# Kernel tuning notes

Measured on AMD Instinct MI355X. Metric: run time of the kernel, lower is better.

The kernel has to match this reference:

```python
import jax, jax.numpy as jnp
import numpy as np

N_HEADS = 16
D_MODEL = 1024
D_HEAD = 64
B, S = 4, 2048


def setup_inputs() -> dict:
    key = jax.random.key(0)
    kv, kk, kq, kwi, kwo = jax.random.split(key, 5)
    v = jax.random.normal(kv, (B, S, D_MODEL), dtype=jnp.float32)
    k = jax.random.normal(kk, (B, S, D_MODEL), dtype=jnp.float32)
    q = jax.random.normal(kq, (B, S, D_MODEL), dtype=jnp.float32)
    wi = jax.random.normal(kwi, (D_MODEL, D_HEAD), dtype=jnp.float32) * (D_MODEL ** -0.5)
    Wo = jax.random.normal(kwo, (N_HEADS * D_HEAD, D_MODEL), dtype=jnp.float32) * ((N_HEADS * D_HEAD) ** -0.5)
    bo = jnp.zeros((D_MODEL,), dtype=jnp.float32)
    return {"v": v, "k": k, "q": q, "wi": wi, "Wo": Wo, "bo": bo}


def reference(v, k, q, wi, Wo, bo):
    # Every head shares the same wi and has no params -> all head outputs are identical.
    # Compute the single head once, then tile n_heads times (matches jnp.concatenate of copies).
    qp = q @ wi  # [B,S,Dh]
    kp = k @ wi
    vp = v @ wi
    scores = jnp.einsum("bsd,btd->bst", qp, kp) / jnp.sqrt(jnp.asarray(D_HEAD, qp.dtype))
    attn = jax.nn.softmax(scores, axis=-1)  # [B,S,S]
    head = qp + jnp.einsum("bst,btd->bsd", attn, vp)  # residual q + attn@v, [B,S,Dh]
    concat = jnp.tile(head, (1, 1, N_HEADS))  # [B,S,n_heads*Dh]
    return concat @ Wo + bo  # Dense(d_model)
```

## Files before the change

kernel.cpp:

```cpp
#include <hip/hip_runtime.h>

typedef __bf16 bf16x8 __attribute__((ext_vector_type(8)));
typedef float f32x4 __attribute__((ext_vector_type(4)));
typedef unsigned short ushort8 __attribute__((ext_vector_type(8)));
typedef unsigned short ushort4v __attribute__((ext_vector_type(4)));

#define S_LEN 2048
#define DMODEL 1024
#define DHEAD 64
#define QK_SCALE 0.18033688f

static __device__ __forceinline__ unsigned short f2bf(float x) {
  __bf16 h = (__bf16)x;
  return __builtin_bit_cast(unsigned short, h);
}

static __device__ __forceinline__ f32x4 mfma16(bf16x8 a, bf16x8 b, f32x4 c) {
  return __builtin_amdgcn_mfma_f32_16x16x32_bf16(a, b, c, 0, 0, 0);
}

#define GLOAD_LDS(SRC, DST)                                                            \
  __builtin_amdgcn_global_load_lds(                                                    \
      (const __attribute__((address_space(1))) void*)(SRC),                            \
      (__attribute__((address_space(3))) void*)(DST), 16, 0, 0)

__global__ void prep_kernel(const float* __restrict__ wi, const float* __restrict__ Wo,
                            unsigned short* __restrict__ wiT,
                            unsigned short* __restrict__ wosumT) {
  int i = blockIdx.x * 256 + threadIdx.x;
  if (i < 65536) {
    int n = i >> 10, kk = i & 1023;
    wiT[i] = f2bf(wi[(size_t)kk * DHEAD + n]);
  } else {
    int idx = i - 65536;
    int j = idx & 1023, d = idx >> 10;
    float s = 0.f;
#pragma unroll
    for (int h = 0; h < 16; ++h) s += Wo[(size_t)(h * 64 + d) * 1024 + j];
    wosumT[(size_t)j * 64 + d] = f2bf(s);
  }
}

__global__ __launch_bounds__(64) void proj_kernel(
    const float* __restrict__ q, const float* __restrict__ k, const float* __restrict__ v,
    const unsigned short* __restrict__ wiT,
    float* __restrict__ qp32, unsigned short* __restrict__ qp_bf,
    unsigned short* __restrict__ kp_bf, unsigned short* __restrict__ vpT) {
  int bx = blockIdx.x;
  int ten = bx >> 9;
  int m0 = (bx & 511) << 4;
  const float* x = (ten == 0) ? q : ((ten == 1) ? k : v);
  int lane = threadIdx.x;
  int l15 = lane & 15, lg = lane >> 4;

  __shared__ __align__(16) char As[4 * 2048];
  __shared__ __align__(16) char Bs[4 * 4096];
  __shared__ __align__(16) unsigned short vt[16][72];

  const char* xb = (const char*)x;
  const char* wb = (const char*)wiT;

  const char* pA0 = xb + (size_t)(m0 + (lane >> 3)) * 4096 + ((((lane & 7) ^ (lane >> 3))) << 4);
  const char* pA1 = pA0 + 8 * 4096;
  const char* pB = wb + (size_t)(lane >> 2) * 2048 + ((((lane & 3) ^ ((lane >> 2) & 3))) << 4);

  auto ISSUE = [&](int st) {
    int buf = st & 3;
    char* ad = As + buf * 2048;
    char* bd = Bs + buf * 4096;
    GLOAD_LDS(pA0 + st * 128, ad);
    GLOAD_LDS(pA1 + st * 128, ad + 1024);
#pragma unroll
    for (int j = 0; j < 4; ++j) GLOAD_LDS(pB + j * 32768 + st * 64, bd + j * 1024);
  };

  f32x4 acc[4] = {};
  int swA = (l15 & 7) << 4;
  int swB = (l15 & 3) << 4;

  auto COMP = [&](int kt) {
    const char* Ab = As + (kt & 3) * 2048 + l15 * 128;
    f32x4 a0 = *(const f32x4*)(Ab + ((lg * 32) ^ swA));
    f32x4 a1 = *(const f32x4*)(Ab + ((lg * 32 + 16) ^ swA));
    bf16x8 af;
    af[0] = (__bf16)a0[0]; af[1] = (__bf16)a0[1]; af[2] = (__bf16)a0[2]; af[3] = (__bf16)a0[3];
    af[4] = (__bf16)a1[0]; af[5] = (__bf16)a1[1]; af[6] = (__bf16)a1[2]; af[7] = (__bf16)a1[3];
    const char* Bb = Bs + (kt & 3) * 4096 + ((lg * 16) ^ swB) + l15 * 64;
#pragma unroll
    for (int t = 0; t < 4; ++t) {
      bf16x8 bfr = *(const bf16x8*)(Bb + t * 1024);
      acc[t] = mfma16(af, bfr, acc[t]);
    }
  };

  ISSUE(0);
  ISSUE(1);
  ISSUE(2);
#pragma unroll 1
  for (int kt = 0; kt < 29; ++kt) {
    ISSUE(kt + 3);
    asm volatile("s_waitcnt vmcnt(18)" ::: "memory");
    __builtin_amdgcn_sched_barrier(0);
    COMP(kt);
    __builtin_amdgcn_sched_barrier(0);
  }
  asm volatile("s_waitcnt vmcnt(12)" ::: "memory");
  __builtin_amdgcn_sched_barrier(0);
  COMP(29);
  asm volatile("s_waitcnt vmcnt(6)" ::: "memory");
  __builtin_amdgcn_sched_barrier(0);
  COMP(30);
  asm volatile("s_waitcnt vmcnt(0)" ::: "memory");
  __builtin_amdgcn_sched_barrier(0);
  COMP(31);

  if (ten == 2) {
#pragma unroll
    for (int t = 0; t < 4; ++t)
#pragma unroll
      for (int r = 0; r < 4; ++r)
        vt[lg * 4 + r][t * 16 + l15] = f2bf(acc[t][r]);
    __syncthreads();
    int bq = m0 >> 11, kvb = m0 & 2047;
    unsigned short* dst = vpT + (size_t)bq * 131072 + (size_t)(kvb >> 6) * 4096 +
                          (size_t)lane * 64 + (kvb & 63);
    ushort8 o0, o1;
#pragma unroll
    for (int j = 0; j < 8; ++j) {
      o0[j] = vt[j][lane];
      o1[j] = vt[8 + j][lane];
    }
    *(ushort8*)dst = o0;
    *(ushort8*)(dst + 8) = o1;
  } else {
#pragma unroll
    for (int t = 0; t < 4; ++t) {
      int gc = t * 16 + l15;
#pragma unroll
      for (int r = 0; r < 4; ++r) {
        size_t idx = (size_t)(m0 + lg * 4 + r) * DHEAD + gc;
        float val = acc[t][r];
        if (ten == 0) {
          qp32[idx] = val;
          qp_bf[idx] = f2bf(val * QK_SCALE);
        } else {
          kp_bf[idx] = f2bf(val);
        }
      }
    }
  }
}

__global__ __launch_bounds__(256, 2) void attn_out_kernel(
    const unsigned short* __restrict__ qp_bf, const unsigned short* __restrict__ kp_bf,
    const unsigned short* __restrict__ vpT, const float* __restrict__ qp32,
    const unsigned short* __restrict__ wosumT, const float* __restrict__ bo,
    float* __restrict__ out) {
  int bx = blockIdx.x;
  int b = bx >> 7;
  int q0 = (bx & 127) << 4;
  int tid = threadIdx.x, lane = tid & 63, w = tid >> 6;
  int l15 = lane & 15, lg = lane >> 4;
  int r8 = lane >> 3, c8 = lane & 7;

  __shared__ __align__(16) char smem[74752];
  char* Kt = smem + w * 16384;
  char* Vt = Kt + 8192;
  unsigned short(*P_w)[72] = (unsigned short(*)[72])(smem + 65536 + w * 2304);
  float* part_w = (float*)Kt;
  float* lsum_w = (float*)(Kt + 4096);
  unsigned short(*head_lds)[72] = (unsigned short(*)[72])(smem + 65536);

  size_t base = (size_t)b * (S_LEN * DHEAD);
  const unsigned short* qrow_p = qp_bf + base + (size_t)(q0 + l15) * DHEAD + lg * 8;
  bf16x8 qf0 = *(const bf16x8*)qrow_p;
  bf16x8 qf1 = *(const bf16x8*)(qrow_p + 32);

  const char* pK = (const char*)(kp_bf + base) + r8 * 128 + ((c8 ^ r8) << 4);
  const char* pV = (const char*)vpT + (size_t)b * 262144 + r8 * 128 + ((c8 ^ r8) << 4);

  auto KISSUE = [&](int it2) {
    const char* s = pK + (size_t)(w * 512 + it2 * 64) * 128;
#pragma unroll
    for (int j = 0; j < 8; ++j) GLOAD_LDS(s + j * 1024, Kt + j * 1024);
  };
  auto VISSUE = [&](int it2) {
    const char* s = pV + (size_t)(w * 8 + it2) * 8192;
#pragma unroll
    for (int j = 0; j < 8; ++j) GLOAD_LDS(s + j * 1024, Vt + j * 1024);
  };

  f32x4 oacc[4] = {};
  float lsum_p = 0.f;
  int swz = (l15 & 7) << 4;

  KISSUE(0);
  VISSUE(0);
#pragma unroll
  for (int it = 0; it < 8; ++it) {
    asm volatile("s_waitcnt vmcnt(8)" ::: "memory");
    __builtin_amdgcn_sched_barrier(0);
    f32x4 sc[4];
#pragma unroll
    for (int sub = 0; sub < 4; ++sub) {
      const char* kr = Kt + (sub * 16 + l15) * 128;
      bf16x8 kf0 = *(const bf16x8*)(kr + ((lg * 16) ^ swz));
      bf16x8 kf1 = *(const bf16x8*)(kr + ((64 + lg * 16) ^ swz));
      f32x4 z = {};
      z = mfma16(kf0, qf0, z);
      sc[sub] = mfma16(kf1, qf1, z);
    }
    asm volatile("s_waitcnt lgkmcnt(0)" ::: "memory");
    __builtin_amdgcn_sched_barrier(0);
    if (it < 7) KISSUE(it + 1);
#pragma unroll
    for (int sub = 0; sub < 4; ++sub) {
      ushort4v pw;
#pragma unroll
      for (int r = 0; r < 4; ++r) {
        float p = exp2f(sc[sub][r]);
        lsum_p += p;
        pw[r] = f2bf(p);
      }
      *(ushort4v*)&P_w[l15][sub * 16 + lg * 4] = pw;
    }
    if (it < 7) {
      asm volatile("s_waitcnt vmcnt(8)" ::: "memory");
    } else {
      asm volatile("s_waitcnt vmcnt(0)" ::: "memory");
    }
    __builtin_amdgcn_sched_barrier(0);
#pragma unroll
    for (int c = 0; c < 2; ++c) {
      bf16x8 pf = *(const bf16x8*)&P_w[l15][c * 32 + lg * 8];
#pragma unroll
      for (int t = 0; t < 4; ++t) {
        const char* vr = Vt + (t * 16 + l15) * 128;
        bf16x8 vf = *(const bf16x8*)(vr + ((c * 64 + lg * 16) ^ swz));
        oacc[t] = mfma16(pf, vf, oacc[t]);
      }
    }
    asm volatile("s_waitcnt lgkmcnt(0)" ::: "memory");
    __builtin_amdgcn_sched_barrier(0);
    if (it < 7) VISSUE(it + 1);
  }

  lsum_p += __shfl_xor(lsum_p, 16);
  lsum_p += __shfl_xor(lsum_p, 32);

#pragma unroll
  for (int t = 0; t < 4; ++t)
#pragma unroll
    for (int r = 0; r < 4; ++r)
      part_w[(lg * 4 + r) * 64 + t * 16 + l15] = oacc[t][r];
  if (lane < 16) lsum_w[l15] = lsum_p;
  __syncthreads();

  {
    int qr = tid >> 4, d0 = (tid & 15) << 2;
    f32x4 s = *(const f32x4*)(smem + 0 * 16384 + (qr * 64 + d0) * 4);
    s += *(const f32x4*)(smem + 1 * 16384 + (qr * 64 + d0) * 4);
    s += *(const f32x4*)(smem + 2 * 16384 + (qr * 64 + d0) * 4);
    s += *(const f32x4*)(smem + 3 * 16384 + (qr * 64 + d0) * 4);
    float l = ((float*)(smem + 0 * 16384 + 4096))[qr] + ((float*)(smem + 1 * 16384 + 4096))[qr] +
              ((float*)(smem + 2 * 16384 + 4096))[qr] + ((float*)(smem + 3 * 16384 + 4096))[qr];
    float inv = 1.0f / l;
    size_t idx = base + (size_t)(q0 + qr) * DHEAD + d0;
    f32x4 qv = *(const f32x4*)(qp32 + idx);
    f32x4 res = qv + s * inv;
    ushort4v hb;
#pragma unroll
    for (int j = 0; j < 4; ++j) hb[j] = f2bf(res[j]);
    *(ushort4v*)&head_lds[qr][d0] = hb;
  }
  __syncthreads();

  bf16x8 af0 = *(const bf16x8*)&head_lds[l15][lg * 8];
  bf16x8 af1 = *(const bf16x8*)&head_lds[l15][32 + lg * 8];
  size_t orow = ((size_t)b * S_LEN + q0 + lg * 4) * 1024;
  int c0 = w * 256;
#pragma unroll
  for (int t = 0; t < 16; ++t) {
    int col = c0 + t * 16 + l15;
    const unsigned short* bp = wosumT + (size_t)col * 64 + lg * 8;
    bf16x8 b0 = *(const bf16x8*)bp;
    bf16x8 b1 = *(const bf16x8*)(bp + 32);
    f32x4 acc = {};
    acc = mfma16(af0, b0, acc);
    acc = mfma16(af1, b1, acc);
    float bias = bo[col];
#pragma unroll
    for (int r = 0; r < 4; ++r) out[orow + (size_t)r * 1024 + col] = acc[r] + bias;
  }
}

extern "C" void kernel_launch(void* const* d_in, const int* in_sizes, int n_in,
                              void* d_out, int out_size, void* d_ws, size_t ws_size,
                              hipStream_t stream) {
  (void)in_sizes; (void)n_in; (void)out_size; (void)ws_size;
  const float* v = (const float*)d_in[0];
  const float* k = (const float*)d_in[1];
  const float* q = (const float*)d_in[2];
  const float* wi = (const float*)d_in[3];
  const float* Wo = (const float*)d_in[4];
  const float* bo = (const float*)d_in[5];
  float* out = (float*)d_out;
  char* ws = (char*)d_ws;

  float* qp32 = (float*)(ws + 0);
  unsigned short* qp_bf = (unsigned short*)(ws + (4u << 20));
  unsigned short* kp_bf = (unsigned short*)(ws + (5u << 20));
  unsigned short* vpT = (unsigned short*)(ws + (6u << 20));
  unsigned short* wiT = (unsigned short*)(ws + (7u << 20));
  unsigned short* wosumT = (unsigned short*)(ws + (7u << 20) + (512u << 10));

  prep_kernel<<<512, 256, 0, stream>>>(wi, Wo, wiT, wosumT);
  proj_kernel<<<1536, 64, 0, stream>>>(q, k, v, wiT, qp32, qp_bf, kp_bf, vpT);
  attn_out_kernel<<<512, 256, 0, stream>>>(qp_bf, kp_bf, vpT, qp32, wosumT, bo, out);
}
```

Baseline: 57.34 us.

## Double-buffer K/V tiles with 32-key chunks and new V^T layout

Splits each wave's key range into 16 chunks of 32 keys instead of 8 chunks of 64, and double-buffers both K and V tiles in LDS so the next-next chunk's loads are in flight during compute. The transposed V projection is rewritten in 32-key blocks with a matching swizzle so each V tile is contiguous 4KB. The aim is to hide global-to-LDS latency better and trim LDS use slightly. In exchange there are more loop iterations and waitcnt points, and smaller MFMA batches per iteration.

```diff
diff --git a/kernel.cpp b/kernel.cpp
--- a/kernel.cpp
+++ b/kernel.cpp
@@ -122,8 +122,8 @@
         vt[lg * 4 + r][t * 16 + l15] = f2bf(acc[t][r]);
     __syncthreads();
     int bq = m0 >> 11, kvb = m0 & 2047;
-    unsigned short* dst = vpT + (size_t)bq * 131072 + (size_t)(kvb >> 6) * 4096 +
-                          (size_t)lane * 64 + (kvb & 63);
+    unsigned short* dst = vpT + (size_t)bq * 131072 + (size_t)(kvb >> 5) * 2048 +
+                          (size_t)lane * 32 + (kvb & 31);
     ushort8 o0, o1;
 #pragma unroll
     for (int j = 0; j < 8; ++j) {
@@ -163,12 +163,14 @@
   int l15 = lane & 15, lg = lane >> 4;
   int r8 = lane >> 3, c8 = lane & 7;
 
-  __shared__ __align__(16) char smem[74752];
-  char* Kt = smem + w * 16384;
-  char* Vt = Kt + 8192;
-  unsigned short(*P_w)[72] = (unsigned short(*)[72])(smem + 65536 + w * 2304);
-  float* part_w = (float*)Kt;
-  float* lsum_w = (float*)(Kt + 4096);
+  __shared__ __align__(16) char smem[70656];
+  char* Kt0 = smem + w * 16384;
+  char* Kt1 = Kt0 + 4096;
+  char* Vt0 = Kt0 + 8192;
+  char* Vt1 = Kt0 + 12288;
+  unsigned short* P_w = (unsigned short*)(smem + 65536 + w * 1280);
+  float* part_w = (float*)Kt0;
+  float* lsum_w = (float*)Vt0;
   unsigned short(*head_lds)[72] = (unsigned short(*)[72])(smem + 65536);
 
   size_t base = (size_t)b * (S_LEN * DHEAD);
@@ -176,45 +178,56 @@
   bf16x8 qf0 = *(const bf16x8*)qrow_p;
   bf16x8 qf1 = *(const bf16x8*)(qrow_p + 32);
 
-  const char* pK = (const char*)(kp_bf + base) + r8 * 128 + ((c8 ^ r8) << 4);
-  const char* pV = (const char*)vpT + (size_t)b * 262144 + r8 * 128 + ((c8 ^ r8) << 4);
-
-  auto KISSUE = [&](int it2) {
-    const char* s = pK + (size_t)(w * 512 + it2 * 64) * 128;
-#pragma unroll
-    for (int j = 0; j < 8; ++j) GLOAD_LDS(s + j * 1024, Kt + j * 1024);
+  const char* pK = (const char*)(kp_bf + base) + r8 * 128 + ((c8 ^ r8) << 4) +
+                   (size_t)w * 512 * 128;
+  const char* pV = (const char*)vpT + (size_t)b * 262144 + (lane >> 2) * 64 +
+                   ((((lane & 3) ^ ((lane >> 2) & 3))) << 4) + (size_t)w * 16 * 4096;
+
+  auto KISSUE = [&](int it2, char* dstK) {
+    const char* s = pK + (size_t)it2 * 4096;
+#pragma unroll
+    for (int j = 0; j < 4; ++j) GLOAD_LDS(s + j * 1024, dstK + j * 1024);
   };
-  auto VISSUE = [&](int it2) {
-    const char* s = pV + (size_t)(w * 8 + it2) * 8192;
-#pragma unroll
-    for (int j = 0; j < 8; ++j) GLOAD_LDS(s + j * 1024, Vt + j * 1024);
+  auto VISSUE = [&](int it2, char* dstV) {
+    const char* s = pV + (size_t)it2 * 4096;
+#pragma unroll
+    for (int j = 0; j < 4; ++j) GLOAD_LDS(s + j * 1024, dstV + j * 1024);
   };
 
   f32x4 oacc[4] = {};
   float lsum_p = 0.f;
-  int swz = (l15 & 7) << 4;
-
-  KISSUE(0);
-  VISSUE(0);
-#pragma unroll
-  for (int it = 0; it < 8; ++it) {
-    asm volatile("s_waitcnt vmcnt(8)" ::: "memory");
-    __builtin_amdgcn_sched_barrier(0);
-    f32x4 sc[4];
-#pragma unroll
-    for (int sub = 0; sub < 4; ++sub) {
-      const char* kr = Kt + (sub * 16 + l15) * 128;
-      bf16x8 kf0 = *(const bf16x8*)(kr + ((lg * 16) ^ swz));
-      bf16x8 kf1 = *(const bf16x8*)(kr + ((64 + lg * 16) ^ swz));
+  int swzK = (l15 & 7) << 4;
+  int swzV = (l15 & 3);
+
+  KISSUE(0, Kt0);
+  VISSUE(0, Vt0);
+  KISSUE(1, Kt1);
+  VISSUE(1, Vt1);
+#pragma unroll
+  for (int it = 0; it < 16; ++it) {
+    char* Kc = (it & 1) ? Kt1 : Kt0;
+    char* Vc = (it & 1) ? Vt1 : Vt0;
+    if (it < 15) {
+      asm volatile("s_waitcnt vmcnt(12)" ::: "memory");
+    } else {
+      asm volatile("s_waitcnt vmcnt(4)" ::: "memory");
+    }
+    __builtin_amdgcn_sched_barrier(0);
+    f32x4 sc[2];
+#pragma unroll
+    for (int sub = 0; sub < 2; ++sub) {
+      const char* kr = Kc + (sub * 16 + l15) * 128;
+      bf16x8 kf0 = *(const bf16x8*)(kr + ((lg * 16) ^ swzK));
+      bf16x8 kf1 = *(const bf16x8*)(kr + ((64 + lg * 16) ^ swzK));
       f32x4 z = {};
       z = mfma16(kf0, qf0, z);
       sc[sub] = mfma16(kf1, qf1, z);
     }
     asm volatile("s_waitcnt lgkmcnt(0)" ::: "memory");
     __builtin_amdgcn_sched_barrier(0);
-    if (it < 7) KISSUE(it + 1);
-#pragma unroll
-    for (int sub = 0; sub < 4; ++sub) {
+    if (it < 14) KISSUE(it + 2, Kc);
+#pragma unroll
+    for (int sub = 0; sub < 2; ++sub) {
       ushort4v pw;
 #pragma unroll
       for (int r = 0; r < 4; ++r) {
@@ -222,27 +235,27 @@
         lsum_p += p;
         pw[r] = f2bf(p);
       }
-      *(ushort4v*)&P_w[l15][sub * 16 + lg * 4] = pw;
-    }
-    if (it < 7) {
+      *(ushort4v*)(P_w + l15 * 40 + sub * 16 + lg * 4) = pw;
+    }
+    if (it < 14) {
+      asm volatile("s_waitcnt vmcnt(12)" ::: "memory");
+    } else if (it == 14) {
       asm volatile("s_waitcnt vmcnt(8)" ::: "memory");
     } else {
       asm volatile("s_waitcnt vmcnt(0)" ::: "memory");
     }
     __builtin_amdgcn_sched_barrier(0);
-#pragma unroll
-    for (int c = 0; c < 2; ++c) {
-      bf16x8 pf = *(const bf16x8*)&P_w[l15][c * 32 + lg * 8];
-#pragma unroll
-      for (int t = 0; t < 4; ++t) {
-        const char* vr = Vt + (t * 16 + l15) * 128;
-        bf16x8 vf = *(const bf16x8*)(vr + ((c * 64 + lg * 16) ^ swz));
-        oacc[t] = mfma16(pf, vf, oacc[t]);
-      }
+    bf16x8 pf = *(const bf16x8*)(P_w + l15 * 40 + lg * 8);
+#pragma unroll
+    for (int t = 0; t < 4; ++t) {
+      int vrow = t * 16 + l15;
+      const char* vr = Vc + vrow * 64 + (((lg ^ swzV)) << 4);
+      bf16x8 vf = *(const bf16x8*)vr;
+      oacc[t] = mfma16(pf, vf, oacc[t]);
     }
     asm volatile("s_waitcnt lgkmcnt(0)" ::: "memory");
     __builtin_amdgcn_sched_barrier(0);
-    if (it < 7) VISSUE(it + 1);
+    if (it < 14) VISSUE(it + 2, Vc);
   }
 
   lsum_p += __shfl_xor(lsum_p, 16);
@@ -262,8 +275,8 @@
     s += *(const f32x4*)(smem + 1 * 16384 + (qr * 64 + d0) * 4);
     s += *(const f32x4*)(smem + 2 * 16384 + (qr * 64 + d0) * 4);
     s += *(const f32x4*)(smem + 3 * 16384 + (qr * 64 + d0) * 4);
-    float l = ((float*)(smem + 0 * 16384 + 4096))[qr] + ((float*)(smem + 1 * 16384 + 4096))[qr] +
-              ((float*)(smem + 2 * 16384 + 4096))[qr] + ((float*)(smem + 3 * 16384 + 4096))[qr];
+    float l = ((float*)(smem + 0 * 16384 + 8192))[qr] + ((float*)(smem + 1 * 16384 + 8192))[qr] +
+              ((float*)(smem + 2 * 16384 + 8192))[qr] + ((float*)(smem + 3 * 16384 + 8192))[qr];
     float inv = 1.0f / l;
     size_t idx = base + (size_t)(q0 + qr) * DHEAD + d0;
     f32x4 qv = *(const f32x4*)(qp32 + idx);
```

Measured after the change: 57.21 us. No clear change (-0.2%).
